# Kernel tuning notes

Measured on AMD Instinct MI355X. Metric: run time of the kernel, lower is better.

## Reference

```python
import jax, jax.numpy as jnp
import numpy as np

B, R, C, O, I = 256, 1152, 10, 16, 8  # batch, routes, digit caps, out dim, in dim


def conv2d(x, w, b, stride, pad):
    y = jax.lax.conv_general_dilated(
        x, w, (stride, stride), ((pad, pad), (pad, pad)),
        dimension_numbers=("NCHW", "OIHW", "NCHW"))
    return y + b[None, :, None, None]


def maxpool2(x):
    # kernel 2, stride 2, padding 1 (torch pads with -inf for max pool)
    return jax.lax.reduce_window(
        x, -jnp.inf, jax.lax.max,
        (1, 1, 2, 2), (1, 1, 2, 2), ((0, 0), (0, 0), (1, 1), (1, 1)))


def squash(t):
    sn = (t ** 2).sum(-1, keepdims=True)
    return sn * t / ((1.0 + sn) * jnp.sqrt(sn))


def setup_inputs() -> dict:
    key = jax.random.key(0)
    ks = jax.random.split(key, 8)
    return {
        "data": jax.random.normal(ks[0], (B, 3, 76, 76), dtype=jnp.float32),
        "conv1_w": jax.random.normal(ks[1], (64, 3, 3, 3), dtype=jnp.float32) * 0.1,
        "conv1_b": jnp.zeros((64,), jnp.float32),
        "conv2_w": jax.random.normal(ks[2], (128, 64, 3, 3), dtype=jnp.float32) * 0.05,
        "conv2_b": jnp.zeros((128,), jnp.float32),
        "prim_w": jax.random.normal(ks[3], (8, 32, 128, 9, 9), dtype=jnp.float32) * 0.02,
        "prim_b": jnp.zeros((8, 32), jnp.float32),
        "W": jax.random.normal(ks[4], (R, C, O, I), dtype=jnp.float32),
        "cls_w1": jax.random.normal(ks[5], (10, 160, 100), dtype=jnp.float32) * 0.05,
        "cls_b1": jnp.zeros((10, 100), jnp.float32),
        "cls_w2": jax.random.normal(ks[6], (10, 100, 1), dtype=jnp.float32) * 0.05,
        "cls_b2": jnp.zeros((10, 1), jnp.float32),
    }


def reference(data, conv1_w, conv1_b, conv2_w, conv2_b, prim_w, prim_b, W,
              cls_w1, cls_b1, cls_w2, cls_b2):
    # ---- ConvLayer ----
    x = jax.nn.relu(conv2d(data, conv1_w, conv1_b, 1, 0))   # [B,64,74,74]
    x = maxpool2(x)                                          # [B,64,38,38]
    x = jax.nn.relu(conv2d(x, conv2_w, conv2_b, 1, 1))       # [B,128,38,38]
    x = maxpool2(x)                                          # [B,128,20,20]

    # ---- PrimaryCaps: 8 parallel convs fused into one grouped-by-output conv ----
    pw = prim_w.reshape(8 * 32, 128, 9, 9)
    pb = prim_b.reshape(8 * 32)
    u = conv2d(x, pw, pb, 2, 0)                              # [B,256,6,6]
    u = u.reshape(B, R, I)                                   # [B,1152,8] (same flatten order as torch view)
    u = squash(u)

    # ---- DigitCaps dynamic routing ----
    u_hat = jnp.einsum("rcoi,bri->brco", W, u)               # [B,R,C,O]
    b_ij = jnp.zeros((R, C), u_hat.dtype)
    v_j = None
    for it in range(3):
        c_ij = jax.nn.softmax(b_ij, axis=0)                  # softmax over routes (dim=1 in torch)
        s_j = jnp.einsum("rc,brco->bco", c_ij, u_hat)        # [B,C,O]
        # torch squashes over trailing singleton dim -> elementwise squash
        v_j = squash(s_j[..., None])[..., 0]                 # [B,C,O]
        if it < 2:
            a_ij = jnp.einsum("brco,bco->brc", u_hat, v_j).mean(0)  # [R,C]
            b_ij = b_ij + a_ij

    output = v_j[..., None]                                  # [B,10,16,1]

    # ---- 10 classifiers (Linear->ReLU->Linear->Sigmoid), batched over classifier idx k ----
    feat = output.reshape(B, -1)                             # [B,160]
    h = jax.nn.relu(jnp.einsum("bf,kfh->bkh", feat, cls_w1) + cls_b1)
    logits = jnp.einsum("bkh,kho->bko", h, cls_w2) + cls_b2  # [B,10,1]
    cls = jax.nn.sigmoid(logits)[..., 0]                     # [B,10]
    return (output, cls)
```

## Files before the change

kernel.cpp:

```cpp
#include <hip/hip_runtime.h>
#include <hip/hip_bf16.h>


typedef __bf16 bf16x8 __attribute__((ext_vector_type(8)));
typedef float  f32x4  __attribute__((ext_vector_type(4)));
typedef ushort u16x8  __attribute__((ext_vector_type(8)));

static __device__ __forceinline__ ushort f2bf(float f) {
    __hip_bfloat16 h = __float2bfloat16(f);
    return *(ushort*)&h;
}
static __device__ __forceinline__ float b2f(ushort u) {
    return __uint_as_float(((unsigned)u) << 16);
}

typedef __attribute__((address_space(1))) const unsigned int* as1_u32p;
typedef __attribute__((address_space(3))) unsigned int* as3_u32p;
static __device__ __forceinline__ void gl16(const void* g, void* l) {
    __builtin_amdgcn_global_load_lds((as1_u32p)g, (as3_u32p)l, 16, 0, 0);
}

__global__ __launch_bounds__(256) void k_prep_all(
    const float* __restrict__ w1, const float* __restrict__ w2,
    const float* __restrict__ pw, const float* __restrict__ W,
    __hip_bfloat16* __restrict__ Aw1, __hip_bfloat16* __restrict__ Aw2,
    __hip_bfloat16* __restrict__ Awt, __hip_bfloat16* __restrict__ Wt)
{
    int t = blockIdx.x * 256 + threadIdx.x;
    if (t < 2654208) {
        int oc = t / 10368, rem = t % 10368;
        int k81 = rem >> 7, ic = rem & 127;
        Awt[t] = __float2bfloat16(pw[(oc * 128 + ic) * 81 + k81]);
    } else if (t < 4128768) {
        int q = t - 2654208;
        int k = q / 160, co = q % 160;
        int r = k >> 3, i = k & 7, c = co >> 4, o = co & 15;
        Wt[q] = __float2bfloat16(W[(((size_t)r * 10 + c) * 16 + o) * 8 + i]);
    } else if (t < 4202496) {
        int q = t - 4128768;
        int oc = q / 576, rem = q % 576;
        int k9 = rem >> 6, ic = rem & 63;
        Aw2[q] = __float2bfloat16(w2[(oc * 64 + ic) * 9 + k9]);
    } else {
        int q = t - 4202496;
        int oc = q >> 5, k = q & 31;
        Aw1[q] = __float2bfloat16(k < 27 ? w1[oc * 27 + k] : 0.f);
    }
}

__global__ __launch_bounds__(256) void k_conv1_mfma(
    const float* __restrict__ data, const __hip_bfloat16* __restrict__ Aw1,
    const float* __restrict__ b1, __hip_bfloat16* __restrict__ P1t)
{
    __shared__ float tile[960];
    const int tid = threadIdx.x;
    const int py = blockIdx.x % 38, b = blockIdx.x / 38;

    #pragma unroll
    for (int c = 0; c < 4; c++) {
        int idx = tid + c * 256;
        if (idx < 960) {
            float val = 0.f;
            if (idx < 936) {
                int ic = idx / 312, rem = idx % 312;
                int rl = rem / 78, lc = rem % 78;
                int ri = 2 * py - 1 + rl, xi = lc - 1;
                if ((unsigned)ri < 76u && (unsigned)xi < 76u)
                    val = data[(b * 3 + ic) * 5776 + ri * 76 + xi];
            }
            tile[idx] = val;
        }
    }

    const int wave = tid >> 6, lane = tid & 63;
    const int l15 = lane & 15, quad = lane >> 4;

    bf16x8 af = *(const bf16x8*)((const ushort*)Aw1 + (wave * 16 + l15) * 32 + quad * 8);

    int koff[8]; bool kok[8];
    #pragma unroll
    for (int j = 0; j < 8; j++) {
        int kk = quad * 8 + j;
        kok[j] = kk < 27;
        int ic = kk / 9, rem = kk - ic * 9, ky = rem / 3, kx = rem - ky * 3;
        koff[j] = kok[j] ? (ic * 312 + ky * 78 + kx) : 0;
    }

    float bias[4];
    #pragma unroll
    for (int r = 0; r < 4; r++) bias[r] = b1[wave * 16 + quad * 4 + r];

    const bool valid0 = (py > 0);
    const bool valid1 = (py < 37);

    __syncthreads();

    #pragma unroll
    for (int t5 = 0; t5 < 5; t5++) {
        int n_x = t5 * 16 + l15;
        bool col_ok = (unsigned)(n_x - 1) < 74u;

        bf16x8 bf0, bf1;
        #pragma unroll
        for (int j = 0; j < 8; j++) {
            float v0 = tile[koff[j] + n_x];
            float v1 = tile[koff[j] + 78 + n_x];
            bool ok = col_ok && kok[j];
            bf0[j] = (__bf16)(ok ? v0 : 0.f);
            bf1[j] = (__bf16)(ok ? v1 : 0.f);
        }
        f32x4 z = {0.f, 0.f, 0.f, 0.f};
        f32x4 c0 = __builtin_amdgcn_mfma_f32_16x16x32_bf16(af, bf0, z, 0, 0, 0);
        f32x4 c1 = __builtin_amdgcn_mfma_f32_16x16x32_bf16(af, bf1, z, 0, 0, 0);

        f32x4 p;
        #pragma unroll
        for (int r = 0; r < 4; r++) {
            float r0 = (valid0 && col_ok) ? fmaxf(c0[r] + bias[r], 0.f) : 0.f;
            float r1 = (valid1 && col_ok) ? fmaxf(c1[r] + bias[r], 0.f) : 0.f;
            p[r] = fmaxf(r0, r1);
        }
        #pragma unroll
        for (int r = 0; r < 4; r++)
            p[r] = fmaxf(p[r], __shfl_xor(p[r], 1));

        if (!(l15 & 1)) {
            int px = t5 * 8 + (l15 >> 1);
            if (px < 38) {
                ushort4 pk;
                pk.x = f2bf(p[0]); pk.y = f2bf(p[1]);
                pk.z = f2bf(p[2]); pk.w = f2bf(p[3]);
                *(ushort4*)((ushort*)P1t + ((size_t)(b * 38 + py) * 38 + px) * 64
                            + wave * 16 + quad * 4) = pk;
            }
        }
    }
}

__global__ __launch_bounds__(256, 4) void k_conv2_pool_mfma(
    const __hip_bfloat16* __restrict__ P1t,
    const __hip_bfloat16* __restrict__ Aw2,
    const float* __restrict__ cb,
    __hip_bfloat16* __restrict__ P2t)
{
    __shared__ ushort lA[128 * 64];
    __shared__ ushort lB[128 * 64];
    const int tid  = threadIdx.x;
    const int grp  = blockIdx.x / 50, toff = blockIdx.x % 50;
    const int wave = tid >> 6, lane = tid & 63;
    const int wm   = wave & 1, wn = wave >> 1;
    const int lane15 = lane & 15, quad = lane >> 4;

    const int sl = ((lane & 7) ^ (lane >> 3)) * 8;

    int oA[4], oB[4];
    #pragma unroll
    for (int i = 0; i < 4; i++) {
        int row = wave * 32 + i * 8 + (lane >> 3);
        oA[i] = row * 576 + sl;
        int off = toff * 128 + row;
        int bb = off / 1600, rem = off % 1600;
        int cell = rem >> 2, q = rem & 3;
        int py = cell / 20, px = cell % 20;
        int y = 2 * py - 1 + (q >> 1), x = 2 * px - 1 + (q & 1);
        int b = grp * 4 + bb;
        oB[i] = (((b * 38 + (y - 1)) * 38 + (x - 1)) << 6) + sl;
    }
    ushort* lAq = &lA[wave * 2048];
    ushort* lBq = &lB[wave * 2048];

    const int s7 = lane15 & 7;
    const int c0 = (quad ^ s7) * 8;
    const int c1 = ((quad + 4) ^ s7) * 8;
    const ushort* aRd0 = &lA[(wm * 64 + lane15) * 64 + c0];
    const ushort* aRd1 = &lA[(wm * 64 + lane15) * 64 + c1];
    const ushort* bRd0 = &lB[(wn * 64 + lane15) * 64 + c0];
    const ushort* bRd1 = &lB[(wn * 64 + lane15) * 64 + c1];

    f32x4 zero = {0.f, 0.f, 0.f, 0.f};
    f32x4 acc[4][4];
    #pragma unroll
    for (int i = 0; i < 4; i++)
        #pragma unroll
        for (int j = 0; j < 4; j++) acc[i][j] = zero;

    for (int kb = 0; kb < 9; kb++) {
        int ky = kb / 3, kx = kb - ky * 3;
        int dB = (ky * 38 + kx) << 6;
        int dA = kb << 6;

        __syncthreads();
        #pragma unroll
        for (int i = 0; i < 4; i++) {
            gl16(Aw2 + oA[i] + dA, lAq + i * 512);
            gl16(P1t + (ptrdiff_t)(oB[i] + dB), lBq + i * 512);
        }
        __syncthreads();

        #pragma unroll
        for (int kk = 0; kk < 2; kk++) {
            const ushort* ap = kk ? aRd1 : aRd0;
            const ushort* bp = kk ? bRd1 : bRd0;
            bf16x8 af[4], bf[4];
            #pragma unroll
            for (int tm = 0; tm < 4; tm++)
                af[tm] = *(const bf16x8*)(ap + tm * 1024);
            #pragma unroll
            for (int tn = 0; tn < 4; tn++)
                bf[tn] = *(const bf16x8*)(bp + tn * 1024);
            #pragma unroll
            for (int tm = 0; tm < 4; tm++)
                #pragma unroll
                for (int tn = 0; tn < 4; tn++)
                    acc[tm][tn] = __builtin_amdgcn_mfma_f32_16x16x32_bf16(
                        af[tm], bf[tn], acc[tm][tn], 0, 0, 0);
        }
    }

    #pragma unroll
    for (int tn = 0; tn < 4; tn++) {
        int woff = toff * 128 + wn * 64 + tn * 16 + lane15;
        int ebb = woff / 1600, erem = woff % 1600;
        int ecell = erem >> 2, eq = erem & 3;
        int epy = ecell / 20, epx = ecell % 20;
        int ey = 2 * epy - 1 + (eq >> 1), ex = 2 * epx - 1 + (eq & 1);
        bool vq = ((unsigned)ey < 38u) && ((unsigned)ex < 38u);
        int eb = grp * 4 + ebb;
        #pragma unroll
        for (int tm = 0; tm < 4; tm++) {
            int m0 = wm * 64 + tm * 16 + quad * 4;
            f32x4 a = acc[tm][tn];
            f32x4 p;
            #pragma unroll
            for (int r = 0; r < 4; r++)
                p[r] = vq ? fmaxf(a[r] + cb[m0 + r], 0.f) : 0.f;
            #pragma unroll
            for (int r = 0; r < 4; r++) {
                p[r] = fmaxf(p[r], __shfl_xor(p[r], 1));
                p[r] = fmaxf(p[r], __shfl_xor(p[r], 2));
            }
            if (eq == 0) {
                ushort4 pk;
                pk.x = f2bf(p[0]); pk.y = f2bf(p[1]);
                pk.z = f2bf(p[2]); pk.w = f2bf(p[3]);
                *(ushort4*)((ushort*)P2t + (((size_t)eb * 20 + epy) * 20 + epx) * 128 + m0) = pk;
            }
        }
    }
}

__global__ __launch_bounds__(256, 4) void k_primcaps_mfma(
    const __hip_bfloat16* __restrict__ P2t,
    const __hip_bfloat16* __restrict__ Awt,
    float* __restrict__ partU)
{
    __shared__ ushort lA[128 * 64];
    __shared__ ushort lB[128 * 64];
    const int tid  = threadIdx.x;
    const int chunk = blockIdx.x / 144;
    const int tile  = blockIdx.x % 144;
    const int bm   = tile & 1;
    const int bn   = tile >> 1;
    const int wave = tid >> 6, lane = tid & 63;
    const int wm   = wave & 1, wn = wave >> 1;
    const int lane15 = lane & 15, quad = lane >> 4;

    const int sl = ((lane & 7) ^ (lane >> 3)) * 8;

    int oA[4], oB[4];
    #pragma unroll
    for (int i = 0; i < 4; i++) {
        int row = wave * 32 + i * 8 + (lane >> 3);
        oA[i] = (bm * 128 + row) * 10368 + sl;
        int n = bn * 128 + row;
        int cbn = n / 36, cs = n % 36;
        int cy = cs / 6, cx = cs % 6;
        oB[i] = ((cbn * 20 + 2 * cy) * 20 + 2 * cx) * 128 + sl;
    }
    ushort* lAq = &lA[wave * 2048];
    ushort* lBq = &lB[wave * 2048];

    const int s7 = lane15 & 7;
    const int c0 = (quad ^ s7) * 8;
    const int c1 = ((quad + 4) ^ s7) * 8;
    const ushort* aRd0 = &lA[(wm * 64 + lane15) * 64 + c0];
    const ushort* aRd1 = &lA[(wm * 64 + lane15) * 64 + c1];
    const ushort* bRd0 = &lB[(wn * 64 + lane15) * 64 + c0];
    const ushort* bRd1 = &lB[(wn * 64 + lane15) * 64 + c1];

    f32x4 zero = {0.f, 0.f, 0.f, 0.f};
    f32x4 acc[4][4];
    #pragma unroll
    for (int i = 0; i < 4; i++)
        #pragma unroll
        for (int j = 0; j < 4; j++) acc[i][j] = zero;

    const int kb0 = chunk * 27;
    for (int ki = 0; ki < 27; ki++) {
        int kb = kb0 + ki;
        int k81 = kb >> 1;
        int ky = k81 / 9, kx = k81 - ky * 9;
        int dB = (ky * 20 + kx) * 128 + (kb & 1) * 64;
        int dA = kb << 6;

        __syncthreads();
        #pragma unroll
        for (int i = 0; i < 4; i++) {
            gl16(Awt + (size_t)(oA[i] + dA), lAq + i * 512);
            gl16(P2t + (oB[i] + dB), lBq + i * 512);
        }
        __syncthreads();

        #pragma unroll
        for (int kk = 0; kk < 2; kk++) {
            const ushort* ap = kk ? aRd1 : aRd0;
            const ushort* bp = kk ? bRd1 : bRd0;
            bf16x8 af[4], bf[4];
            #pragma unroll
            for (int tm = 0; tm < 4; tm++)
                af[tm] = *(const bf16x8*)(ap + tm * 1024);
            #pragma unroll
            for (int tn = 0; tn < 4; tn++)
                bf[tn] = *(const bf16x8*)(bp + tn * 1024);
            #pragma unroll
            for (int tm = 0; tm < 4; tm++)
                #pragma unroll
                for (int tn = 0; tn < 4; tn++)
                    acc[tm][tn] = __builtin_amdgcn_mfma_f32_16x16x32_bf16(
                        af[tm], bf[tn], acc[tm][tn], 0, 0, 0);
        }
    }

    float* base = partU + chunk * 2359296;
    #pragma unroll
    for (int tm = 0; tm < 4; tm++) {
        int m0 = bm * 128 + wm * 64 + tm * 16 + quad * 4;
        #pragma unroll
        for (int tn = 0; tn < 4; tn++) {
            int nn = bn * 128 + wn * 64 + tn * 16 + lane15;
            int ob = nn / 36, os = nn % 36;
            float* up = base + ob * 9216 + os;
            f32x4 a = acc[tm][tn];
            #pragma unroll
            for (int r = 0; r < 4; r++)
                up[(m0 + r) * 36] = a[r];
        }
    }
}

__global__ __launch_bounds__(256) void k_reduce_squash(
    const float* __restrict__ partU, const float* __restrict__ pb,
    ushort* __restrict__ u_bf)
{
    int t = blockIdx.x * 256 + threadIdx.x;
    float4 a = {0.f, 0.f, 0.f, 0.f}, b4 = {0.f, 0.f, 0.f, 0.f};
    #pragma unroll
    for (int p = 0; p < 6; p++) {
        const float4* pp = (const float4*)(partU + p * 2359296 + t * 8);
        float4 x = pp[0], y = pp[1];
        a.x += x.x; a.y += x.y; a.z += x.z; a.w += x.w;
        b4.x += y.x; b4.y += y.y; b4.z += y.z; b4.w += y.w;
    }
    int lb = (t % 1152) * 8;
    int oc0 = lb / 36, s0 = lb - oc0 * 36;
    float vals[8] = {a.x, a.y, a.z, a.w, b4.x, b4.y, b4.z, b4.w};
    float sn = 0.f;
    #pragma unroll
    for (int e = 0; e < 8; e++) {
        int oc = oc0 + ((s0 + e) >= 36 ? 1 : 0);
        vals[e] += pb[oc];
        sn += vals[e] * vals[e];
    }
    float sc = sqrtf(sn) / (1.f + sn);
    u16x8 o8;
    #pragma unroll
    for (int e = 0; e < 8; e++) o8[e] = f2bf(vals[e] * sc);
    *(u16x8*)(u_bf + (size_t)t * 8) = o8;
}

__global__ __launch_bounds__(320) void k_sj_fused(
    const ushort* __restrict__ u_bf,
    const __hip_bfloat16* __restrict__ Wt,
    const float* __restrict__ expb,
    float* __restrict__ partS,
    int iter)
{
    __shared__ ushort ush[8 * 1152];
    __shared__ float cf[1440];
    __shared__ float sred[320];
    __shared__ float sinv[10];
    const int tid = threadIdx.x;
    const int bt = blockIdx.x & 31, kc = blockIdx.x >> 5;
    const int co = tid % 160, half = tid / 160;

    if (iter > 0) {
        int c = tid % 10, g = tid / 10;
        float s = 0.f;
        for (int r = g; r < 1152; r += 32) s += expb[r * 10 + c];
        sred[tid] = s;
        for (int i = tid; i < 1440; i += 320) cf[i] = expb[kc * 1440 + i];
        __syncthreads();
        if (tid < 10) {
            float t2 = 0.f;
            #pragma unroll
            for (int gg = 0; gg < 32; gg++) t2 += sred[tid + gg * 10];
            sinv[tid] = 1.f / t2;
        }
    }
    for (int i = tid; i < 1152; i += 320)
        ((uint4*)ush)[i] = ((const uint4*)u_bf)[(size_t)(bt * 8 + (i / 144)) * 1152
                                                + kc * 144 + (i % 144)];
    __syncthreads();

    const int cc = co >> 4;
    const float scl = (iter > 0) ? sinv[cc] : 0.f;
    const float cuni = 1.f / 1152.f;
    const ushort* wp = (const ushort*)Wt + ((size_t)kc * 1152 + half * 576) * 160 + co;

    float acc[8] = {0.f, 0.f, 0.f, 0.f, 0.f, 0.f, 0.f, 0.f};
    for (int rr = 0; rr < 72; rr++) {
        float cl = (iter == 0) ? cuni : cf[(half * 72 + rr) * 10 + cc] * scl;
        float wv[8];
        #pragma unroll
        for (int ii = 0; ii < 8; ii++)
            wv[ii] = b2f(wp[(rr * 8 + ii) * 160]) * cl;
        int kbase = half * 576 + rr * 8;
        #pragma unroll
        for (int bb = 0; bb < 8; bb++) {
            u16x8 uq = *(const u16x8*)&ush[bb * 1152 + kbase];
            #pragma unroll
            for (int ii = 0; ii < 8; ii++)
                acc[bb] += wv[ii] * b2f(uq[ii]);
        }
    }
    float* ps = partS + (kc * 2 + half) * 40960;
    #pragma unroll
    for (int bb = 0; bb < 8; bb++)
        ps[(bt * 8 + bb) * 160 + co] = acc[bb];
}

__global__ __launch_bounds__(320) void k_vj_cls(
    const float* __restrict__ partS, float* __restrict__ v,
    const float* __restrict__ w1, const float* __restrict__ b1,
    const float* __restrict__ w2, const float* __restrict__ b2,
    float* __restrict__ out, int write_out)
{
    const int b = blockIdx.x;
    const int tid = threadIdx.x;
    __shared__ float feat[160];
    if (tid < 160) {
        float s = 0.f;
        #pragma unroll
        for (int p = 0; p < 16; p++) s += partS[p * 40960 + b * 160 + tid];
        float vv = s * fabsf(s) / (1.f + s * s);
        v[b * 160 + tid] = vv;
        feat[tid] = vv;
        if (write_out) out[b * 160 + tid] = vv;
    }
    if (!write_out) return;
    __syncthreads();
    int k = tid >> 5, j = tid & 31;
    float acc = 0.f;
    for (int h = j; h < 100; h += 32) {
        float a = b1[k * 100 + h];
        for (int f = 0; f < 160; f++) a += feat[f] * w1[(k * 160 + f) * 100 + h];
        acc += fmaxf(a, 0.f) * w2[k * 100 + h];
    }
    #pragma unroll
    for (int d = 16; d > 0; d >>= 1) acc += __shfl_xor(acc, d);
    if (j == 0)
        out[40960 + b * 10 + k] = 1.f / (1.f + expf(-(acc + b2[k])));
}

__global__ __launch_bounds__(320) void k_mmat_aij(
    const ushort* __restrict__ u_bf, const float* __restrict__ v,
    const float* __restrict__ W, float* __restrict__ bij,
    float* __restrict__ expb)
{
    const int r = blockIdx.x;
    const int tid = threadIdx.x;
    const int co = tid % 160, bh = tid / 160;
    float acc[8] = {0.f, 0.f, 0.f, 0.f, 0.f, 0.f, 0.f, 0.f};
    for (int b = bh; b < 256; b += 2) {
        float vv = v[b * 160 + co];
        u16x8 uq = *(const u16x8*)(u_bf + (size_t)b * 9216 + r * 8);
        #pragma unroll
        for (int j = 0; j < 8; j++) acc[j] += vv * b2f(uq[j]);
    }
    __shared__ float red[2560];
    __shared__ float Ml[8][160];
    #pragma unroll
    for (int j = 0; j < 8; j++) red[j * 320 + bh * 160 + co] = acc[j];
    __syncthreads();
    if (tid < 160) {
        #pragma unroll
        for (int j = 0; j < 8; j++)
            Ml[j][tid] = (red[j * 320 + tid] + red[j * 320 + 160 + tid]) * (1.f / 256.f);
    }
    __syncthreads();
    int c = tid >> 5, j32 = tid & 31;
    const float* wr = W + ((size_t)r * 10 + c) * 128;
    float a2 = 0.f;
    #pragma unroll
    for (int m = 0; m < 4; m++) {
        int idx = j32 + m * 32;
        int o = idx >> 3, i = idx & 7;
        a2 += wr[idx] * Ml[i][c * 16 + o];
    }
    #pragma unroll
    for (int d = 16; d > 0; d >>= 1) a2 += __shfl_xor(a2, d);
    if (j32 == 0) {
        float nb = bij[c * 1152 + r] + a2;
        bij[c * 1152 + r] = nb;
        expb[r * 10 + c] = expf(nb);
    }
}

extern "C" void kernel_launch(void* const* d_in, const int* in_sizes, int n_in,
                              void* d_out, int out_size, void* d_ws, size_t ws_size,
                              hipStream_t stream) {
    const float* data    = (const float*)d_in[0];
    const float* conv1_w = (const float*)d_in[1];
    const float* conv1_b = (const float*)d_in[2];
    const float* conv2_w = (const float*)d_in[3];
    const float* conv2_b = (const float*)d_in[4];
    const float* prim_w  = (const float*)d_in[5];
    const float* prim_b  = (const float*)d_in[6];
    const float* W       = (const float*)d_in[7];
    const float* cls_w1  = (const float*)d_in[8];
    const float* cls_b1  = (const float*)d_in[9];
    const float* cls_w2  = (const float*)d_in[10];
    const float* cls_b2  = (const float*)d_in[11];
    float* out = (float*)d_out;

    char* ws = (char*)d_ws;
    float*          partU = (float*)(ws + 0);
    __hip_bfloat16* P2t   = (__hip_bfloat16*)(ws + 56623104);
    __hip_bfloat16* P1t   = (__hip_bfloat16*)(ws + 94633984);
    __hip_bfloat16* Awt   = (__hip_bfloat16*)(ws + 141950976);
    __hip_bfloat16* Wt    = (__hip_bfloat16*)(ws + 147259392);
    ushort*         u_bf  = (ushort*)(ws + 150208512);
    float*          partS = (float*)(ws + 154927104);
    float*          v     = (float*)(ws + 163446784);
    float*          bij   = (float*)(ws + 163610624);
    float*          expb  = (float*)(ws + 163656704);
    __hip_bfloat16* Aw2   = (__hip_bfloat16*)(ws + 163702784);
    __hip_bfloat16* Aw1   = (__hip_bfloat16*)(ws + 163850240);

    hipMemsetAsync(bij, 0, 11520 * sizeof(float), stream);

    k_prep_all<<<16424, 256, 0, stream>>>(conv1_w, conv2_w, prim_w, W,
                                          Aw1, Aw2, Awt, Wt);
    k_conv1_mfma<<<9728, 256, 0, stream>>>(data, Aw1, conv1_b, P1t);
    k_conv2_pool_mfma<<<3200, 256, 0, stream>>>(P1t, Aw2, conv2_b, P2t);
    k_primcaps_mfma<<<864, 256, 0, stream>>>(P2t, Awt, partU);
    k_reduce_squash<<<1152, 256, 0, stream>>>(partU, prim_b, u_bf);

    for (int it = 0; it < 3; it++) {
        k_sj_fused<<<256, 320, 0, stream>>>(u_bf, Wt, expb, partS, it);
        k_vj_cls<<<256, 320, 0, stream>>>(partS, v, cls_w1, cls_b1, cls_w2,
                                          cls_b2, out, it == 2 ? 1 : 0);
        if (it < 2)
            k_mmat_aij<<<1152, 320, 0, stream>>>(u_bf, v, W, bij, expb);
    }
}
```

Before: 569.1 us.

## Double-buffer LDS staging in conv2 and primary-caps MFMA GEMMs

Both MFMA conv kernels now keep two LDS buffers for A and B, so the next K-step's global-to-LDS loads are issued before computing on the current buffer, with one barrier per iteration instead of two. In conv2, out-of-bounds padding reads now point at a small zeroed page in the workspace instead of reading off-image addresses. LDS use doubles to 64KB per block and launch bounds drop to 2 blocks per CU, trading occupancy for overlap of load latency with MFMA work.

New measurement: 628.9 us. 1.11x slower.

```diff
diff --git a/kernel.cpp b/kernel.cpp
--- a/kernel.cpp
+++ b/kernel.cpp
@@ -137,14 +137,15 @@
     }
 }
 
-__global__ __launch_bounds__(256, 4) void k_conv2_pool_mfma(
+__global__ __launch_bounds__(256, 2) void k_conv2_pool_mfma(
     const __hip_bfloat16* __restrict__ P1t,
     const __hip_bfloat16* __restrict__ Aw2,
     const float* __restrict__ cb,
+    const ushort* __restrict__ zpage,
     __hip_bfloat16* __restrict__ P2t)
 {
-    __shared__ ushort lA[128 * 64];
-    __shared__ ushort lB[128 * 64];
+    __shared__ ushort lA[2][128 * 64];
+    __shared__ ushort lB[2][128 * 64];
     const int tid  = threadIdx.x;
     const int grp  = blockIdx.x / 50, toff = blockIdx.x % 50;
     const int wave = tid >> 6, lane = tid & 63;
@@ -153,7 +154,7 @@
 
     const int sl = ((lane & 7) ^ (lane >> 3)) * 8;
 
-    int oA[4], oB[4];
+    int oA[4], oB[4], yv[4], xv[4];
     #pragma unroll
     for (int i = 0; i < 4; i++) {
         int row = wave * 32 + i * 8 + (lane >> 3);
@@ -163,19 +164,16 @@
         int cell = rem >> 2, q = rem & 3;
         int py = cell / 20, px = cell % 20;
         int y = 2 * py - 1 + (q >> 1), x = 2 * px - 1 + (q & 1);
-        int b = grp * 4 + bb;
-        oB[i] = (((b * 38 + (y - 1)) * 38 + (x - 1)) << 6) + sl;
-    }
-    ushort* lAq = &lA[wave * 2048];
-    ushort* lBq = &lB[wave * 2048];
+        yv[i] = y; xv[i] = x;
+        oB[i] = (((grp * 4 + bb) * 38 + (y - 1)) * 38 + (x - 1)) * 64 + sl;
+    }
+    const int lws = wave * 2048;
 
     const int s7 = lane15 & 7;
     const int c0 = (quad ^ s7) * 8;
     const int c1 = ((quad + 4) ^ s7) * 8;
-    const ushort* aRd0 = &lA[(wm * 64 + lane15) * 64 + c0];
-    const ushort* aRd1 = &lA[(wm * 64 + lane15) * 64 + c1];
-    const ushort* bRd0 = &lB[(wn * 64 + lane15) * 64 + c0];
-    const ushort* bRd1 = &lB[(wn * 64 + lane15) * 64 + c1];
+    const int aro = (wm * 64 + lane15) * 64;
+    const int bro = (wn * 64 + lane15) * 64;
 
     f32x4 zero = {0.f, 0.f, 0.f, 0.f};
     f32x4 acc[4][4];
@@ -184,23 +182,30 @@
         #pragma unroll
         for (int j = 0; j < 4; j++) acc[i][j] = zero;
 
-    for (int kb = 0; kb < 9; kb++) {
+    auto stage = [&](int kb, int sel) {
         int ky = kb / 3, kx = kb - ky * 3;
         int dB = (ky * 38 + kx) << 6;
         int dA = kb << 6;
-
+        #pragma unroll
+        for (int i = 0; i < 4; i++) {
+            gl16((const ushort*)Aw2 + oA[i] + dA, &lA[sel][lws + i * 512]);
+            bool ok = ((unsigned)(yv[i] - 1 + ky) < 38u) &&
+                      ((unsigned)(xv[i] - 1 + kx) < 38u);
+            const ushort* src = ok ? ((const ushort*)P1t + (ptrdiff_t)(oB[i] + dB))
+                                   : (zpage + sl);
+            gl16(src, &lB[sel][lws + i * 512]);
+        }
+    };
+
+    stage(0, 0);
+    for (int kb = 0; kb < 9; kb++) {
         __syncthreads();
-        #pragma unroll
-        for (int i = 0; i < 4; i++) {
-            gl16(Aw2 + oA[i] + dA, lAq + i * 512);
-            gl16(P1t + (ptrdiff_t)(oB[i] + dB), lBq + i * 512);
-        }
-        __syncthreads();
-
+        if (kb < 8) stage(kb + 1, (kb + 1) & 1);
+        const int sel = kb & 1;
         #pragma unroll
         for (int kk = 0; kk < 2; kk++) {
-            const ushort* ap = kk ? aRd1 : aRd0;
-            const ushort* bp = kk ? bRd1 : bRd0;
+            const ushort* ap = &lA[sel][aro + (kk ? c1 : c0)];
+            const ushort* bp = &lB[sel][bro + (kk ? c1 : c0)];
             bf16x8 af[4], bf[4];
             #pragma unroll
             for (int tm = 0; tm < 4; tm++)
@@ -249,13 +254,13 @@
     }
 }
 
-__global__ __launch_bounds__(256, 4) void k_primcaps_mfma(
+__global__ __launch_bounds__(256, 2) void k_primcaps_mfma(
     const __hip_bfloat16* __restrict__ P2t,
     const __hip_bfloat16* __restrict__ Awt,
     float* __restrict__ partU)
 {
-    __shared__ ushort lA[128 * 64];
-    __shared__ ushort lB[128 * 64];
+    __shared__ ushort lA[2][128 * 64];
+    __shared__ ushort lB[2][128 * 64];
     const int tid  = threadIdx.x;
     const int chunk = blockIdx.x / 144;
     const int tile  = blockIdx.x % 144;
@@ -277,16 +282,13 @@
         int cy = cs / 6, cx = cs % 6;
         oB[i] = ((cbn * 20 + 2 * cy) * 20 + 2 * cx) * 128 + sl;
     }
-    ushort* lAq = &lA[wave * 2048];
-    ushort* lBq = &lB[wave * 2048];
+    const int lws = wave * 2048;
 
     const int s7 = lane15 & 7;
     const int c0 = (quad ^ s7) * 8;
     const int c1 = ((quad + 4) ^ s7) * 8;
-    const ushort* aRd0 = &lA[(wm * 64 + lane15) * 64 + c0];
-    const ushort* aRd1 = &lA[(wm * 64 + lane15) * 64 + c1];
-    const ushort* bRd0 = &lB[(wn * 64 + lane15) * 64 + c0];
-    const ushort* bRd1 = &lB[(wn * 64 + lane15) * 64 + c1];
+    const int aro = (wm * 64 + lane15) * 64;
+    const int bro = (wn * 64 + lane15) * 64;
 
     f32x4 zero = {0.f, 0.f, 0.f, 0.f};
     f32x4 acc[4][4];
@@ -296,25 +298,29 @@
         for (int j = 0; j < 4; j++) acc[i][j] = zero;
 
     const int kb0 = chunk * 27;
-    for (int ki = 0; ki < 27; ki++) {
+
+    auto stage = [&](int ki, int sel) {
         int kb = kb0 + ki;
         int k81 = kb >> 1;
         int ky = k81 / 9, kx = k81 - ky * 9;
         int dB = (ky * 20 + kx) * 128 + (kb & 1) * 64;
         int dA = kb << 6;
-
+        #pragma unroll
+        for (int i = 0; i < 4; i++) {
+            gl16((const ushort*)Awt + (size_t)oA[i] + dA, &lA[sel][lws + i * 512]);
+            gl16((const ushort*)P2t + oB[i] + dB, &lB[sel][lws + i * 512]);
+        }
+    };
+
+    stage(0, 0);
+    for (int ki = 0; ki < 27; ki++) {
         __syncthreads();
-        #pragma unroll
-        for (int i = 0; i < 4; i++) {
-            gl16(Awt + (size_t)(oA[i] + dA), lAq + i * 512);
-            gl16(P2t + (oB[i] + dB), lBq + i * 512);
-        }
-        __syncthreads();
-
+        if (ki < 26) stage(ki + 1, (ki + 1) & 1);
+        const int sel = ki & 1;
         #pragma unroll
         for (int kk = 0; kk < 2; kk++) {
-            const ushort* ap = kk ? aRd1 : aRd0;
-            const ushort* bp = kk ? bRd1 : bRd0;
+            const ushort* ap = &lA[sel][aro + (kk ? c1 : c0)];
+            const ushort* bp = &lB[sel][bro + (kk ? c1 : c0)];
             bf16x8 af[4], bf[4];
             #pragma unroll
             for (int tm = 0; tm < 4; tm++)
@@ -536,6 +542,7 @@
     char* ws = (char*)d_ws;
     float*          partU = (float*)(ws + 0);
     __hip_bfloat16* P2t   = (__hip_bfloat16*)(ws + 56623104);
+    ushort*         zpage = (ushort*)(ws + 69730304);
     __hip_bfloat16* P1t   = (__hip_bfloat16*)(ws + 94633984);
     __hip_bfloat16* Awt   = (__hip_bfloat16*)(ws + 141950976);
     __hip_bfloat16* Wt    = (__hip_bfloat16*)(ws + 147259392);
@@ -548,11 +555,12 @@
     __hip_bfloat16* Aw1   = (__hip_bfloat16*)(ws + 163850240);
 
     hipMemsetAsync(bij, 0, 11520 * sizeof(float), stream);
+    hipMemsetAsync(zpage, 0, 128, stream);
 
     k_prep_all<<<16424, 256, 0, stream>>>(conv1_w, conv2_w, prim_w, W,
                                           Aw1, Aw2, Awt, Wt);
     k_conv1_mfma<<<9728, 256, 0, stream>>>(data, Aw1, conv1_b, P1t);
-    k_conv2_pool_mfma<<<3200, 256, 0, stream>>>(P1t, Aw2, conv2_b, P2t);
+    k_conv2_pool_mfma<<<3200, 256, 0, stream>>>(P1t, Aw2, conv2_b, zpage, P2t);
     k_primcaps_mfma<<<864, 256, 0, stream>>>(P2t, Awt, partU);
     k_reduce_squash<<<1152, 256, 0, stream>>>(partU, prim_b, u_bf);
 
```
